# Kernel optimization log

Hardware: AMD Instinct MI355X
Metric: run time of the kernel (lower is better)

## Reference

```python
import jax, jax.numpy as jnp
import numpy as np

B, R, C = 4, 36, 3          # batch, n_rotations, kernel_dim/output_dim
H, W = 384, 224             # padded image spatial: (320+64, 160+64)
CROP = 64
PAD = CROP // 2             # pad_size = 32


def setup_inputs() -> dict:
    key = jax.random.key(0)
    k1, k2 = jax.random.split(key)
    logits = jax.random.normal(k1, (B, C, H, W), dtype=jnp.float32)
    kernel = jax.random.normal(k2, (B * R, C, CROP, CROP), dtype=jnp.float32)
    return {"logits": logits, "kernel": kernel}


def _correlate(logits, kernel):
    # Original computes a full B x (B*R) cross-correlation via F.conv2d and then
    # discards all off-diagonal blocks. A grouped conv (feature_group_count=B)
    # computes exactly the kept diagonal blocks: group i correlates sample i's
    # feature map with that sample's R rotated kernels. interpolate/crop are
    # per-channel/per-pixel so they commute with the channel selection -> same math.
    b, c, h, w = logits.shape
    r = kernel.shape[0] // b
    x = logits.reshape(1, b * c, h, w)
    out = jax.lax.conv_general_dilated(
        x, kernel,
        window_strides=(1, 1),
        padding=[(PAD, PAD), (PAD, PAD)],
        dimension_numbers=("NCHW", "OIHW", "NCHW"),
        feature_group_count=b,
    )  # [1, b*r, h+1, w+1]  (h + 2*PAD - CROP + 1 = h + 1)
    out = out.reshape(b, r, out.shape[-2], out.shape[-1])
    # F.interpolate(..., mode='bilinear', align_corners=False) == half-pixel
    # bilinear resize without antialiasing.
    out = jax.image.resize(out, (b, r, h, w), method="bilinear", antialias=False)
    out = out[:, :, PAD:-PAD, PAD:-PAD]  # [b, r, h-2*PAD, w-2*PAD] = [b, r, 320, 160]
    hc, wc = out.shape[-2], out.shape[-1]
    # softmax over the flattened per-sample (rotation x spatial) map
    flat = jax.nn.softmax(out.reshape(b, -1), axis=-1)
    return flat.reshape(b, r, hc, wc)


def reference(logits, kernel):
    return _correlate(logits, kernel)
```

## Files before the change

### kernel.cpp

```cpp
#include <hip/hip_runtime.h>

typedef short bf16x8 __attribute__((ext_vector_type(8)));
typedef float f32x4  __attribute__((ext_vector_type(4)));
typedef unsigned short u16;

#define B_ 4
#define R_ 36
#define RP 48
#define C_ 3
#define H_ 384
#define W_ 224
#define KS 64
#define OY 321
#define OX 161
#define HC 320
#define WC 160
#define LCOLS 128
#define PITCH 120
#define GR 3072
#define BLKS_PER_BATCH 7200

__device__ __forceinline__ u16 bf16rtn(float v) {
    union { float f; unsigned u; } U; U.f = v;
    unsigned r = U.u + 0x7fffu + ((U.u >> 16) & 1u);
    return (u16)(r >> 16);
}
__device__ __forceinline__ float bf16tof(u16 h) {
    union { float f; unsigned u; } U; U.u = ((unsigned)h) << 16; return U.f;
}

__device__ __forceinline__ float wave_max(float v) {
    #pragma unroll
    for (int off = 32; off > 0; off >>= 1) v = fmaxf(v, __shfl_down(v, off, 64));
    return v;
}
__device__ __forceinline__ float wave_sum(float v) {
    #pragma unroll
    for (int off = 32; off > 0; off >>= 1) v += __shfl_down(v, off, 64);
    return v;
}

__global__ __launch_bounds__(256) void prep_weights(
    const float* __restrict__ wk, u16* __restrict__ wa)
{
    int d = blockIdx.x * 256 + threadIdx.x;
    int ky32  = d & 31;
    int t1    = d >> 5;
    int r     = t1 % 48;
    int t2    = t1 / 48;
    int plane = t2 & 1;
    int g2    = t2 >> 1;
    int kycp  = g2 & 1;
    int kx    = (g2 >> 1) & 63;
    int bc    = g2 >> 7;
    int c     = bc % 3;
    int b     = bc / 3;
    int ky    = kycp*32 + ky32;
    float v = 0.f;
    if (r < R_) v = wk[(((size_t)(b*R_ + r)*C_ + c)*KS + ky)*KS + kx];
    u16 h = bf16rtn(v);
    u16 o = plane ? bf16rtn(v - bf16tof(h)) : h;
    wa[(size_t)g2*GR + plane*1536 + r*32 + (ky32 ^ (((r >> 1) & 3) << 3))] = o;
}

template<int NT>
__device__ __forceinline__ void conv_body(
    const float* __restrict__ in, const u16* __restrict__ wa,
    float* __restrict__ out, u16* Lh, u16* Ll, int x0, int y0)
{
    const int b    = blockIdx.z;
    const int t    = threadIdx.x;
    const int w    = __builtin_amdgcn_readfirstlane(t >> 6);
    const int lane = t & 63;
    const int nu   = lane & 15;
    const int q    = lane >> 4;

    f32x4 acc[2][3][NT];
    #pragma unroll
    for (int yi = 0; yi < 2; yi++)
        #pragma unroll
        for (int mi = 0; mi < 3; mi++)
            #pragma unroll
            for (int n = 0; n < NT; n++)
                acc[yi][mi][n] = (f32x4){0.f, 0.f, 0.f, 0.f};

    const u16* gbase = wa + (size_t)(b*384)*GR;

    const int sw   = (8*q) ^ (((nu >> 1) & 3) << 3);
    const int offH = nu*32 + sw;

    bf16x8 A0h[3], A0l[3], A1h[3], A1l[3];

    #pragma unroll
    for (int mi = 0; mi < 3; mi++) {
        A0h[mi] = *(const bf16x8*)(gbase + offH + mi*512);
        A0l[mi] = *(const bf16x8*)(gbase + 1536 + offH + mi*512);
    }

#define STEP(G, CH, CL, NH, NL) do {                                         \
    int gn_ = (G) + 1; if (gn_ > 383) gn_ = 383;                             \
    const u16* gp_ = gbase + (size_t)gn_ * GR;                               \
    _Pragma("unroll")                                                        \
    for (int mi = 0; mi < 3; mi++) {                                         \
        NH[mi] = *(const bf16x8*)(gp_ + offH + mi*512);                      \
        NL[mi] = *(const bf16x8*)(gp_ + 1536 + offH + mi*512);               \
    }                                                                        \
    const int kx_   = ((G) & 127) >> 1;                                      \
    const int kycp_ = (G) & 1;                                               \
    const u16* cb_ = Lh + (size_t)(nu + kx_)*PITCH + 32*kycp_ + 8*q + 8*w;   \
    _Pragma("unroll")                                                        \
    for (int n = 0; n < NT; n++) {                                           \
        _Pragma("unroll")                                                    \
        for (int yi = 0; yi < 2; yi++) {                                     \
            const u16* ph_ = cb_ + n*16*PITCH + 32*yi;                       \
            bf16x8 Bh_ = *(const bf16x8*)ph_;                                \
            bf16x8 Bl_ = *(const bf16x8*)(ph_ + (size_t)LCOLS*PITCH);        \
            _Pragma("unroll")                                                \
            for (int mi = 0; mi < 3; mi++) {                                 \
                acc[yi][mi][n] = __builtin_amdgcn_mfma_f32_16x16x32_bf16(CH[mi], Bh_, acc[yi][mi][n], 0, 0, 0); \
                acc[yi][mi][n] = __builtin_amdgcn_mfma_f32_16x16x32_bf16(CH[mi], Bl_, acc[yi][mi][n], 0, 0, 0); \
                acc[yi][mi][n] = __builtin_amdgcn_mfma_f32_16x16x32_bf16(CL[mi], Bh_, acc[yi][mi][n], 0, 0, 0); \
            }                                                                \
        }                                                                    \
    }                                                                        \
} while (0)

    for (int c = 0; c < C_; c++) {
        __syncthreads();
        const float* src = in + ((size_t)(b*C_ + c))*H_*W_;
        #pragma unroll
        for (int k = 0; k < 8; k++) {
            int idx = t + 256*k;
            if (idx < 1920) {
                int a    = idx & 31;
                int pr   = (idx >> 5) + ((a >> 3) & 3);
                if (pr >= 60) pr -= 60;
                int r0   = pr * 2;
                int c4   = a * 4;
                int gx   = x0 + c4;
                int gy   = y0 + r0;
                float4 va = make_float4(0.f,0.f,0.f,0.f), vb = va;
                if (gx < W_) {
                    if (gy < H_)     va = *(const float4*)(src + (size_t)gy*W_ + gx);
                    if (gy + 1 < H_) vb = *(const float4*)(src + (size_t)(gy+1)*W_ + gx);
                }
                const float* pa = &va.x;
                const float* pb = &vb.x;
                #pragma unroll
                for (int j = 0; j < 4; j++) {
                    int col = c4 + j;
                    u16 ha = bf16rtn(pa[j]);
                    u16 hb = bf16rtn(pb[j]);
                    u16 la = bf16rtn(pa[j] - bf16tof(ha));
                    u16 lb = bf16rtn(pb[j] - bf16tof(hb));
                    *(unsigned*)&Lh[col*PITCH + r0] = (unsigned)ha | ((unsigned)hb << 16);
                    *(unsigned*)&Ll[col*PITCH + r0] = (unsigned)la | ((unsigned)lb << 16);
                }
            }
        }
        __syncthreads();

        #pragma unroll 1
        for (int gi2 = 0; gi2 < 128; gi2 += 2) {
            const int g = c*128 + gi2;
            STEP(g,     A0h, A0l, A1h, A1l);
            STEP(g + 1, A1h, A1l, A0h, A0l);
        }
    }
#undef STEP

    #pragma unroll
    for (int yi = 0; yi < 2; yi++) {
        const int y = y0 + 8*w + 32*yi;
        if (y <= 320) {
            #pragma unroll
            for (int mi = 0; mi < 3; mi++) {
                #pragma unroll
                for (int n = 0; n < NT; n++) {
                    #pragma unroll
                    for (int i = 0; i < 4; i++) {
                        int r = mi*16 + q*4 + i;
                        int x = x0 + n*16 + nu;
                        if (r < R_ && x < OX)
                            out[((size_t)(b*R_ + r)*OY + y)*OX + x] = acc[yi][mi][n][i];
                    }
                }
            }
        }
    }
}

__global__ __launch_bounds__(256) void conv_mfma(
    const float* __restrict__ in, const u16* __restrict__ wa, float* __restrict__ out)
{
    __shared__ __align__(16) u16 smem[2*LCOLS*PITCH];
    u16* Lh = smem;
    u16* Ll = smem + LCOLS*PITCH;
    const int s  = blockIdx.y;
    const int y0 = (s < 40) ? ((s >> 3)*64 + (s & 7)) : 320;

    if (blockIdx.x == 0)      conv_body<4>(in, wa, out, Lh, Ll, 0,   y0);
    else if (blockIdx.x == 1) conv_body<4>(in, wa, out, Lh, Ll, 64,  y0);
    else                      conv_body<3>(in, wa, out, Lh, Ll, 128, y0);
}

__global__ __launch_bounds__(256) void resize_kernel(
    const float* __restrict__ cv, float* __restrict__ out, float* __restrict__ pmax)
{
    const int t = threadIdx.x;
    const int idx = blockIdx.x * 256 + t;
    const int j = idx % WC;
    const int rest = idx / WC;
    const int i = rest % HC;
    const int br = rest / HC;

    float fy = (i + 32.5f) * (1.0f/384.0f);
    float fx = (j + 32.5f) * (1.0f/224.0f);

    const float* p = cv + ((size_t)br*OY + i)*OX + j;
    float v00 = p[0], v01 = p[1], v10 = p[OX], v11 = p[OX+1];
    float v = (1.f-fy)*((1.f-fx)*v00 + fx*v01) + fy*((1.f-fx)*v10 + fx*v11);
    out[idx] = v;

    __shared__ float sm[4];
    float m = wave_max(v);
    if ((t & 63) == 0) sm[t >> 6] = m;
    __syncthreads();
    if (t == 0) pmax[blockIdx.x] = fmaxf(fmaxf(sm[0], sm[1]), fmaxf(sm[2], sm[3]));
}

__global__ __launch_bounds__(256) void reduce_kernel(
    const float* __restrict__ part, float* __restrict__ res, int n, int is_sum)
{
    const int b = blockIdx.x;
    const int t = threadIdx.x;
    const float* p = part + (size_t)b*n;
    float v = is_sum ? 0.f : -3.0e38f;
    for (int k = t; k < n; k += 256) v = is_sum ? (v + p[k]) : fmaxf(v, p[k]);
    __shared__ float sm[4];
    float w = is_sum ? wave_sum(v) : wave_max(v);
    if ((t & 63) == 0) sm[t >> 6] = w;
    __syncthreads();
    if (t == 0) {
        res[b] = is_sum ? (sm[0]+sm[1]+sm[2]+sm[3])
                        : fmaxf(fmaxf(sm[0], sm[1]), fmaxf(sm[2], sm[3]));
    }
}

__global__ __launch_bounds__(256) void exp_kernel(
    float* __restrict__ out, const float* __restrict__ bmax, float* __restrict__ psum)
{
    const int t = threadIdx.x;
    const int idx = blockIdx.x * 256 + t;
    const int b = blockIdx.x / BLKS_PER_BATCH;
    float e = expf(out[idx] - bmax[b]);
    out[idx] = e;
    __shared__ float sm[4];
    float s = wave_sum(e);
    if ((t & 63) == 0) sm[t >> 6] = s;
    __syncthreads();
    if (t == 0) psum[blockIdx.x] = sm[0]+sm[1]+sm[2]+sm[3];
}

__global__ __launch_bounds__(256) void scale_kernel(
    float* __restrict__ out, const float* __restrict__ bsum)
{
    const int idx = blockIdx.x * 256 + threadIdx.x;
    const int b = blockIdx.x / BLKS_PER_BATCH;
    out[idx] = out[idx] / bsum[b];
}

extern "C" void kernel_launch(void* const* d_in, const int* in_sizes, int n_in,
                              void* d_out, int out_size, void* d_ws, size_t ws_size,
                              hipStream_t stream)
{
    const float* logits = (const float*)d_in[0];
    const float* wk     = (const float*)d_in[1];
    float* out = (float*)d_out;
    char*  wsB = (char*)d_ws;

    float* convOut = (float*)wsB;
    u16*   wa      = (u16*)(wsB + 29768256);
    float* pmax    = (float*)(wsB + 29768256 + 9437184);
    float* psum    = pmax + 28800;
    float* bmax    = psum + 28800;
    float* bsum    = bmax + 8;

    hipLaunchKernelGGL(prep_weights, dim3(18432), dim3(256), 0, stream, wk, wa);
    hipLaunchKernelGGL(conv_mfma,    dim3(3, 41, B_), dim3(256), 0, stream, logits, wa, convOut);
    hipLaunchKernelGGL(resize_kernel, dim3(28800), dim3(256), 0, stream, convOut, out, pmax);
    hipLaunchKernelGGL(reduce_kernel, dim3(4),     dim3(256), 0, stream, pmax, bmax, BLKS_PER_BATCH, 0);
    hipLaunchKernelGGL(exp_kernel,    dim3(28800), dim3(256), 0, stream, out, bmax, psum);
    hipLaunchKernelGGL(reduce_kernel, dim3(4),     dim3(256), 0, stream, psum, bsum, BLKS_PER_BATCH, 1);
    hipLaunchKernelGGL(scale_kernel,  dim3(28800), dim3(256), 0, stream, out, bsum);
}
```

Measured before the change: 662.4 us.

## Split conv rows across eight waves and interleave MFMA chains with setprio

The conv block grows from 256 to 512 threads. Each wave now owns a single 8-row group instead of two, which halves the accumulator registers per thread and doubles the waves available to hide latency. Inside each step the MFMA sequence is reordered so two column tiles' accumulator chains alternate, and s_setprio raises wave priority around the MFMA burst. The cost is that each weight fragment is now loaded from global memory by twice as many waves, and the launch bounds change how the compiler allocates registers.

```diff
diff --git a/kernel.cpp b/kernel.cpp
--- a/kernel.cpp
+++ b/kernel.cpp
@@ -75,14 +75,12 @@
     const int nu   = lane & 15;
     const int q    = lane >> 4;
 
-    f32x4 acc[2][3][NT];
+    f32x4 acc[3][NT];
     #pragma unroll
-    for (int yi = 0; yi < 2; yi++)
+    for (int mi = 0; mi < 3; mi++)
         #pragma unroll
-        for (int mi = 0; mi < 3; mi++)
-            #pragma unroll
-            for (int n = 0; n < NT; n++)
-                acc[yi][mi][n] = (f32x4){0.f, 0.f, 0.f, 0.f};
+        for (int n = 0; n < NT; n++)
+            acc[mi][n] = (f32x4){0.f, 0.f, 0.f, 0.f};
 
     const u16* gbase = wa + (size_t)(b*384)*GR;
 
@@ -109,19 +107,42 @@
     const int kycp_ = (G) & 1;                                               \
     const u16* cb_ = Lh + (size_t)(nu + kx_)*PITCH + 32*kycp_ + 8*q + 8*w;   \
     _Pragma("unroll")                                                        \
-    for (int n = 0; n < NT; n++) {                                           \
+    for (int n0 = 0; n0 < NT; n0 += 2) {                                     \
+        const u16* p0_ = cb_ + n0*16*PITCH;                                  \
+        bf16x8 Bh0_ = *(const bf16x8*)p0_;                                   \
+        bf16x8 Bl0_ = *(const bf16x8*)(p0_ + (size_t)LCOLS*PITCH);           \
+        bf16x8 Bh1_ = Bh0_, Bl1_ = Bl0_;                                     \
+        if (n0 + 1 < NT) {                                                   \
+            const u16* p1_ = cb_ + (n0+1)*16*PITCH;                          \
+            Bh1_ = *(const bf16x8*)p1_;                                      \
+            Bl1_ = *(const bf16x8*)(p1_ + (size_t)LCOLS*PITCH);              \
+        }                                                                    \
+        __builtin_amdgcn_s_setprio(1);                                       \
         _Pragma("unroll")                                                    \
-        for (int yi = 0; yi < 2; yi++) {                                     \
-            const u16* ph_ = cb_ + n*16*PITCH + 32*yi;                       \
-            bf16x8 Bh_ = *(const bf16x8*)ph_;                                \
-            bf16x8 Bl_ = *(const bf16x8*)(ph_ + (size_t)LCOLS*PITCH);        \
+        for (int mi = 0; mi < 3; mi++)                                       \
+            acc[mi][n0] = __builtin_amdgcn_mfma_f32_16x16x32_bf16(CH[mi], Bh0_, acc[mi][n0], 0, 0, 0); \
+        if (n0 + 1 < NT) {                                                   \
             _Pragma("unroll")                                                \
-            for (int mi = 0; mi < 3; mi++) {                                 \
-                acc[yi][mi][n] = __builtin_amdgcn_mfma_f32_16x16x32_bf16(CH[mi], Bh_, acc[yi][mi][n], 0, 0, 0); \
-                acc[yi][mi][n] = __builtin_amdgcn_mfma_f32_16x16x32_bf16(CH[mi], Bl_, acc[yi][mi][n], 0, 0, 0); \
-                acc[yi][mi][n] = __builtin_amdgcn_mfma_f32_16x16x32_bf16(CL[mi], Bh_, acc[yi][mi][n], 0, 0, 0); \
-            }                                                                \
+            for (int mi = 0; mi < 3; mi++)                                   \
+                acc[mi][n0+1] = __builtin_amdgcn_mfma_f32_16x16x32_bf16(CH[mi], Bh1_, acc[mi][n0+1], 0, 0, 0); \
         }                                                                    \
+        _Pragma("unroll")                                                    \
+        for (int mi = 0; mi < 3; mi++)                                       \
+            acc[mi][n0] = __builtin_amdgcn_mfma_f32_16x16x32_bf16(CH[mi], Bl0_, acc[mi][n0], 0, 0, 0); \
+        if (n0 + 1 < NT) {                                                   \
+            _Pragma("unroll")                                                \
+            for (int mi = 0; mi < 3; mi++)                                   \
+                acc[mi][n0+1] = __builtin_amdgcn_mfma_f32_16x16x32_bf16(CH[mi], Bl1_, acc[mi][n0+1], 0, 0, 0); \
+        }                                                                    \
+        _Pragma("unroll")                                                    \
+        for (int mi = 0; mi < 3; mi++)                                       \
+            acc[mi][n0] = __builtin_amdgcn_mfma_f32_16x16x32_bf16(CL[mi], Bh0_, acc[mi][n0], 0, 0, 0); \
+        if (n0 + 1 < NT) {                                                   \
+            _Pragma("unroll")                                                \
+            for (int mi = 0; mi < 3; mi++)                                   \
+                acc[mi][n0+1] = __builtin_amdgcn_mfma_f32_16x16x32_bf16(CL[mi], Bh1_, acc[mi][n0+1], 0, 0, 0); \
+        }                                                                    \
+        __builtin_amdgcn_s_setprio(0);                                       \
     }                                                                        \
 } while (0)
 
@@ -129,8 +150,8 @@
         __syncthreads();
         const float* src = in + ((size_t)(b*C_ + c))*H_*W_;
         #pragma unroll
-        for (int k = 0; k < 8; k++) {
-            int idx = t + 256*k;
+        for (int k = 0; k < 4; k++) {
+            int idx = t + 512*k;
             if (idx < 1920) {
                 int a    = idx & 31;
                 int pr   = (idx >> 5) + ((a >> 3) & 3);
@@ -169,9 +190,8 @@
     }
 #undef STEP
 
-    #pragma unroll
-    for (int yi = 0; yi < 2; yi++) {
-        const int y = y0 + 8*w + 32*yi;
+    {
+        const int y = y0 + 8*w;
         if (y <= 320) {
             #pragma unroll
             for (int mi = 0; mi < 3; mi++) {
@@ -182,7 +202,7 @@
                         int r = mi*16 + q*4 + i;
                         int x = x0 + n*16 + nu;
                         if (r < R_ && x < OX)
-                            out[((size_t)(b*R_ + r)*OY + y)*OX + x] = acc[yi][mi][n][i];
+                            out[((size_t)(b*R_ + r)*OY + y)*OX + x] = acc[mi][n][i];
                     }
                 }
             }
@@ -190,7 +210,7 @@
     }
 }
 
-__global__ __launch_bounds__(256) void conv_mfma(
+__global__ __launch_bounds__(512, 4) void conv_mfma(
     const float* __restrict__ in, const u16* __restrict__ wa, float* __restrict__ out)
 {
     __shared__ __align__(16) u16 smem[2*LCOLS*PITCH];
@@ -287,7 +307,7 @@
     float* bsum    = bmax + 8;
 
     hipLaunchKernelGGL(prep_weights, dim3(18432), dim3(256), 0, stream, wk, wa);
-    hipLaunchKernelGGL(conv_mfma,    dim3(3, 41, B_), dim3(256), 0, stream, logits, wa, convOut);
+    hipLaunchKernelGGL(conv_mfma,    dim3(3, 41, B_), dim3(512), 0, stream, logits, wa, convOut);
     hipLaunchKernelGGL(resize_kernel, dim3(28800), dim3(256), 0, stream, convOut, out, pmax);
     hipLaunchKernelGGL(reduce_kernel, dim3(4),     dim3(256), 0, stream, pmax, bmax, BLKS_PER_BATCH, 0);
     hipLaunchKernelGGL(exp_kernel,    dim3(28800), dim3(256), 0, stream, out, bmax, psum);
```

Result: no change. 673.3 us (+1.7%).
